# Optimization experiments

Measured on AMD Instinct MI355X. Metric: run time of the kernel, lower is better.

## Reference

```python
import jax, jax.numpy as jnp
import numpy as np

N = 100000          # nodes
E = 1_600_000       # edges (nnz of sparse adj)
IN_F = 256
OUT_F = 128
DROP_P = 0.2


def setup_inputs() -> dict:
    key = jax.random.key(0)
    k1, k2, k3, k4, k5, k6 = jax.random.split(key, 6)
    return {
        "input": jax.random.normal(k1, (N, IN_F), dtype=jnp.float32),
        "weight": jax.random.normal(k2, (IN_F, OUT_F), dtype=jnp.float32) * 0.05,
        "adj_row": jax.random.randint(k3, (E,), 0, N, dtype=jnp.int32),
        "adj_col": jax.random.randint(k4, (E,), 0, N, dtype=jnp.int32),
        "adj_val": jax.random.uniform(k5, (E,), dtype=jnp.float32),
        "drop_u": jax.random.uniform(k6, (N, IN_F), dtype=jnp.float32),
    }


def reference(input, weight, adj_row, adj_col, adj_val, drop_u):
    # F.dropout(input, p, training=True): zero with prob p, scale survivors by 1/(1-p)
    x = jnp.where(drop_u > DROP_P, input / (1.0 - DROP_P), 0.0)
    # dense projection: [N, in] @ [in, out] -> [N, out]
    support = x @ weight
    # SpMM: out[r] = sum over edges e with row==r of val[e] * support[col[e]]
    gathered = support[adj_col] * adj_val[:, None]          # [E, out]
    output = jax.ops.segment_sum(gathered, adj_row, num_segments=N)  # [N, out]
    return output
```

## Files before the change

### kernel.cpp

```cpp
#include <hip/hip_runtime.h>

#define N_NODES 100000
#define IN_F 256
#define OUT_F 128
#define NB 782
#define CAP 2560
#define TILE 4096

typedef __attribute__((ext_vector_type(8))) short v8s;
typedef __attribute__((ext_vector_type(4))) float v4f;

__device__ __forceinline__ unsigned short f2bf(float f) {
    unsigned int u = __float_as_uint(f);
    u += 0x7fffu + ((u >> 16) & 1u);
    return (unsigned short)(u >> 16);
}
__device__ __forceinline__ float bf2f(unsigned short s) {
    return __uint_as_float((unsigned int)s << 16);
}

__global__ __launch_bounds__(256) void drop_kernel(
    const float* __restrict__ x, const float* __restrict__ u,
    unsigned short* __restrict__ xb, int n4) {
    int i = blockIdx.x * 256 + threadIdx.x;
    int stride = gridDim.x * 256;
    for (; i < n4; i += stride) {
        float4 xi = ((const float4*)x)[i];
        float4 du = ((const float4*)u)[i];
        ushort4 pk;
        pk.x = f2bf(du.x > 0.2f ? xi.x * 1.25f : 0.0f);
        pk.y = f2bf(du.y > 0.2f ? xi.y * 1.25f : 0.0f);
        pk.z = f2bf(du.z > 0.2f ? xi.z * 1.25f : 0.0f);
        pk.w = f2bf(du.w > 0.2f ? xi.w * 1.25f : 0.0f);
        ((ushort4*)xb)[i] = pk;
    }
}

__global__ void wt_kernel(const float* __restrict__ w, unsigned short* __restrict__ bt) {
    int idx = blockIdx.x * 256 + threadIdx.x;
    int k = idx >> 7;
    int n = idx & 127;
    bt[n * IN_F + k] = f2bf(w[idx]);
}

__global__ __launch_bounds__(256) void gemm_kernel(
    const unsigned short* __restrict__ xb, const unsigned short* __restrict__ bt,
    unsigned short* __restrict__ support) {
    __shared__ unsigned short As[128 * 72];
    __shared__ unsigned short Bs[128 * 72];

    const int tid  = threadIdx.x;
    const int lane = tid & 63;
    const int wv   = tid >> 6;
    const int wr   = wv >> 1, wc = wv & 1;
    const long long base = (long long)blockIdx.x * 128;

    v4f acc[4][4] = {};

    for (int k0 = 0; k0 < IN_F; k0 += 64) {
        if (k0) __syncthreads();
        {
            const int row = tid >> 1;
            const int kh  = (tid & 1) * 32;
            long long g = base + row;
            unsigned short* dst = &As[row * 72 + kh];
            if (g < N_NODES) {
                const unsigned short* src = xb + g * IN_F + k0 + kh;
                #pragma unroll
                for (int i = 0; i < 4; ++i)
                    *(v8s*)(dst + i * 8) = *(const v8s*)(src + i * 8);
            } else {
                #pragma unroll
                for (int i = 0; i < 4; ++i)
                    *(v8s*)(dst + i * 8) = (v8s){0,0,0,0,0,0,0,0};
            }
        }
        {
            const int n  = tid >> 1;
            const int kh = (tid & 1) * 32;
            const unsigned short* src = bt + n * IN_F + k0 + kh;
            unsigned short* dst = &Bs[n * 72 + kh];
            #pragma unroll
            for (int i = 0; i < 4; ++i)
                *(v8s*)(dst + i * 8) = *(const v8s*)(src + i * 8);
        }
        __syncthreads();
        #pragma unroll
        for (int ks = 0; ks < 2; ++ks) {
            const int kb = ks * 32 + (lane >> 4) * 8;
            v8s af[4], bf[4];
            #pragma unroll
            for (int t = 0; t < 4; ++t)
                af[t] = *(const v8s*)&As[(wr * 64 + t * 16 + (lane & 15)) * 72 + kb];
            #pragma unroll
            for (int t = 0; t < 4; ++t)
                bf[t] = *(const v8s*)&Bs[(wc * 64 + t * 16 + (lane & 15)) * 72 + kb];
            #pragma unroll
            for (int tm = 0; tm < 4; ++tm)
                #pragma unroll
                for (int tn = 0; tn < 4; ++tn)
                    acc[tm][tn] = __builtin_amdgcn_mfma_f32_16x16x32_bf16(
                        af[tm], bf[tn], acc[tm][tn], 0, 0, 0);
        }
    }
    const int rq = lane >> 4;
    const int cl = lane & 15;
    #pragma unroll
    for (int tm = 0; tm < 4; ++tm) {
        #pragma unroll
        for (int r = 0; r < 4; ++r) {
            long long g = base + wr * 64 + tm * 16 + rq * 4 + r;
            if (g < N_NODES) {
                unsigned short* o = support + g * OUT_F + wc * 64 + cl;
                #pragma unroll
                for (int tn = 0; tn < 4; ++tn)
                    o[tn * 16] = f2bf(acc[tm][tn][r]);
            }
        }
    }
}

__global__ void init_kernel(int* __restrict__ cursor) {
    int i = blockIdx.x * 256 + threadIdx.x;
    if (i < NB) cursor[i * 16] = i * CAP;
}

__global__ __launch_bounds__(256) void scatter_kernel(
    const int* __restrict__ row, const int* __restrict__ col,
    const float* __restrict__ val, int* __restrict__ cursor,
    int2* __restrict__ cv, int E) {
    __shared__ int cnt[1024];
    __shared__ int loc[1024];
    __shared__ int delta[1024];
    __shared__ int tmp[256];
    __shared__ int gd[TILE];
    __shared__ int2 stage[TILE];
    __shared__ int total_s;
    const int tid = threadIdx.x;
    const int base_e = blockIdx.x * TILE;

    for (int i = tid; i < 1024; i += 256) cnt[i] = 0;
    __syncthreads();
    #pragma unroll
    for (int j = 0; j < TILE / 256; ++j) {
        int e = base_e + j * 256 + tid;
        if (e < E) atomicAdd(&cnt[row[e] >> 7], 1);
    }
    __syncthreads();
    int c0 = cnt[4*tid], c1 = cnt[4*tid+1], c2 = cnt[4*tid+2], c3 = cnt[4*tid+3];
    int s = c0 + c1 + c2 + c3;
    tmp[tid] = s;
    __syncthreads();
    #pragma unroll
    for (int d = 1; d < 256; d <<= 1) {
        int t = (tid >= d) ? tmp[tid - d] : 0;
        __syncthreads();
        tmp[tid] += t;
        __syncthreads();
    }
    int excl = tmp[tid] - s;
    loc[4*tid]   = excl;
    loc[4*tid+1] = excl + c0;
    loc[4*tid+2] = excl + c0 + c1;
    loc[4*tid+3] = excl + c0 + c1 + c2;
    if (tid == 255) total_s = tmp[255];
    __syncthreads();
    for (int i = tid; i < NB; i += 256) {
        int c = cnt[i];
        int gbase = 0;
        if (c > 0) gbase = atomicAdd(&cursor[i * 16], c);
        delta[i] = gbase - loc[i];
        cnt[i] = loc[i];
    }
    __syncthreads();
    #pragma unroll
    for (int j = 0; j < TILE / 256; ++j) {
        int e = base_e + j * 256 + tid;
        if (e < E) {
            int r = row[e];
            int b = r >> 7;
            int rank = atomicAdd(&cnt[b], 1);
            stage[rank] = make_int2(col[e] | ((r & 127) << 17), __float_as_int(val[e]));
            gd[rank] = delta[b] + rank;
        }
    }
    __syncthreads();
    int total = total_s;
    for (int i = tid; i < total; i += 256)
        cv[gd[i]] = stage[i];
}

__global__ __launch_bounds__(256) void acc2_kernel(
    const int* __restrict__ cursor, const int2* __restrict__ cv,
    const unsigned short* __restrict__ support, float* __restrict__ out) {
    __shared__ int2 sorted[CAP];
    __shared__ int cnt_s[128];
    __shared__ int start_s[128];
    __shared__ int pos_s[128];
    const int tid = threadIdx.x;
    const int b = blockIdx.x;
    const int e0 = b * CAP;
    const int nE = cursor[b * 16] - e0;

    if (tid < 128) cnt_s[tid] = 0;
    __syncthreads();
    for (int i = tid; i < nE; i += 256)
        atomicAdd(&cnt_s[cv[e0 + i].x >> 17], 1);
    __syncthreads();
    int v = (tid < 128) ? cnt_s[tid] : 0;
    int sc = v;
    if (tid < 128) pos_s[tid] = sc;
    __syncthreads();
    #pragma unroll
    for (int d = 1; d < 128; d <<= 1) {
        int t = (tid >= d && tid < 128) ? pos_s[tid - d] : 0;
        __syncthreads();
        if (tid < 128) pos_s[tid] += t;
        __syncthreads();
    }
    if (tid < 128) {
        int st = pos_s[tid] - v;
        start_s[tid] = st;
        pos_s[tid] = st;
    }
    __syncthreads();
    for (int i = tid; i < nE; i += 256) {
        int2 c = cv[e0 + i];
        int rank = atomicAdd(&pos_s[c.x >> 17], 1);
        sorted[rank] = c;
    }
    __syncthreads();
    const int lane = tid & 63, w = tid >> 6;
    const long long rowbase = (long long)b * 128;
    for (int rr = 0; rr < 32; ++rr) {
        int rl = w * 32 + rr;
        int e = start_s[rl];
        int end = e + cnt_s[rl];
        float a0 = 0.f, a1 = 0.f;
        for (; e < end; e += 4) {
            #pragma unroll
            for (int j = 0; j < 4; ++j) {
                int idx = e + j;
                int ids = min(idx, end - 1);
                int2 c = sorted[ids];
                float vv = (idx < end) ? __int_as_float(c.y) : 0.0f;
                int colv = c.x & 131071;
                unsigned int u = *(const unsigned int*)(support + colv * OUT_F + lane * 2);
                a0 = fmaf(vv, bf2f((unsigned short)(u & 0xffff)), a0);
                a1 = fmaf(vv, bf2f((unsigned short)(u >> 16)), a1);
            }
        }
        long long g = rowbase + rl;
        if (g < N_NODES)
            *(float2*)(out + g * OUT_F + lane * 2) = make_float2(a0, a1);
    }
}

extern "C" void kernel_launch(void* const* d_in, const int* in_sizes, int n_in,
                              void* d_out, int out_size, void* d_ws, size_t ws_size,
                              hipStream_t stream) {
    const float* input   = (const float*)d_in[0];
    const float* weight  = (const float*)d_in[1];
    const int*   adj_row = (const int*)d_in[2];
    const int*   adj_col = (const int*)d_in[3];
    const float* adj_val = (const float*)d_in[4];
    const float* drop_u  = (const float*)d_in[5];
    float* out = (float*)d_out;
    const int E = in_sizes[2];

    char* p = (char*)d_ws;
    unsigned short* bt      = (unsigned short*)p;  p += 65536;
    unsigned short* xb      = (unsigned short*)p;
    int2*           cv      = (int2*)p;            p += (size_t)N_NODES * IN_F * 2;
    unsigned short* support = (unsigned short*)p;  p += (size_t)N_NODES * OUT_F * 2;
    int*            cursor  = (int*)p;

    init_kernel<<<4, 256, 0, stream>>>(cursor);
    drop_kernel<<<2048, 256, 0, stream>>>(input, drop_u, xb, N_NODES * IN_F / 4);
    wt_kernel<<<128, 256, 0, stream>>>(weight, bt);
    gemm_kernel<<<(N_NODES + 127) / 128, 256, 0, stream>>>(xb, bt, support);
    scatter_kernel<<<(E + TILE - 1) / TILE, 256, 0, stream>>>(adj_row, adj_col, adj_val, cursor, cv, E);
    acc2_kernel<<<NB, 256, 0, stream>>>(cursor, cv, support, out);
}
```

Measured before the change: 424.7 us.

## Fuse dropout into GEMM load and split SpMM accumulation across four blocks per bucket

The separate dropout kernel is removed. The GEMM now reads fp32 input and dropout uniforms directly, applies the mask and scale, and packs to bf16 while filling shared memory. This avoids a full bf16 intermediate write and read of the dropped input. The accumulation kernel launches four blocks per 128-row bucket, each handling 32 rows with smaller shared memory and a warp-shuffle scan, which raises parallelism and occupancy. In exchange, each block rereads the whole bucket's edge list and filters it, and the GEMM tile load now issues twice as many fp32 reads.

```diff
diff --git a/kernel.cpp b/kernel.cpp
--- a/kernel.cpp
+++ b/kernel.cpp
@@ -5,6 +5,7 @@
 #define OUT_F 128
 #define NB 782
 #define CAP 2560
+#define QCAP 896
 #define TILE 4096
 
 typedef __attribute__((ext_vector_type(8))) short v8s;
@@ -17,23 +18,6 @@
 }
 __device__ __forceinline__ float bf2f(unsigned short s) {
     return __uint_as_float((unsigned int)s << 16);
-}
-
-__global__ __launch_bounds__(256) void drop_kernel(
-    const float* __restrict__ x, const float* __restrict__ u,
-    unsigned short* __restrict__ xb, int n4) {
-    int i = blockIdx.x * 256 + threadIdx.x;
-    int stride = gridDim.x * 256;
-    for (; i < n4; i += stride) {
-        float4 xi = ((const float4*)x)[i];
-        float4 du = ((const float4*)u)[i];
-        ushort4 pk;
-        pk.x = f2bf(du.x > 0.2f ? xi.x * 1.25f : 0.0f);
-        pk.y = f2bf(du.y > 0.2f ? xi.y * 1.25f : 0.0f);
-        pk.z = f2bf(du.z > 0.2f ? xi.z * 1.25f : 0.0f);
-        pk.w = f2bf(du.w > 0.2f ? xi.w * 1.25f : 0.0f);
-        ((ushort4*)xb)[i] = pk;
-    }
 }
 
 __global__ void wt_kernel(const float* __restrict__ w, unsigned short* __restrict__ bt) {
@@ -44,8 +28,8 @@
 }
 
 __global__ __launch_bounds__(256) void gemm_kernel(
-    const unsigned short* __restrict__ xb, const unsigned short* __restrict__ bt,
-    unsigned short* __restrict__ support) {
+    const float* __restrict__ x, const float* __restrict__ u,
+    const unsigned short* __restrict__ bt, unsigned short* __restrict__ support) {
     __shared__ unsigned short As[128 * 72];
     __shared__ unsigned short Bs[128 * 72];
 
@@ -65,10 +49,19 @@
             long long g = base + row;
             unsigned short* dst = &As[row * 72 + kh];
             if (g < N_NODES) {
-                const unsigned short* src = xb + g * IN_F + k0 + kh;
-                #pragma unroll
-                for (int i = 0; i < 4; ++i)
-                    *(v8s*)(dst + i * 8) = *(const v8s*)(src + i * 8);
+                const float* xs = x + g * IN_F + k0 + kh;
+                const float* us = u + g * IN_F + k0 + kh;
+                #pragma unroll
+                for (int i = 0; i < 8; ++i) {
+                    float4 xi = *(const float4*)(xs + i * 4);
+                    float4 du = *(const float4*)(us + i * 4);
+                    ushort4 pk;
+                    pk.x = f2bf(du.x > 0.2f ? xi.x * 1.25f : 0.0f);
+                    pk.y = f2bf(du.y > 0.2f ? xi.y * 1.25f : 0.0f);
+                    pk.z = f2bf(du.z > 0.2f ? xi.z * 1.25f : 0.0f);
+                    pk.w = f2bf(du.w > 0.2f ? xi.w * 1.25f : 0.0f);
+                    *(ushort4*)(dst + i * 4) = pk;
+                }
             } else {
                 #pragma unroll
                 for (int i = 0; i < 4; ++i)
@@ -193,47 +186,50 @@
 __global__ __launch_bounds__(256) void acc2_kernel(
     const int* __restrict__ cursor, const int2* __restrict__ cv,
     const unsigned short* __restrict__ support, float* __restrict__ out) {
-    __shared__ int2 sorted[CAP];
-    __shared__ int cnt_s[128];
-    __shared__ int start_s[128];
-    __shared__ int pos_s[128];
+    __shared__ int2 sorted[QCAP];
+    __shared__ int cnt_s[32];
+    __shared__ int start_s[32];
+    __shared__ int pos_s[32];
     const int tid = threadIdx.x;
-    const int b = blockIdx.x;
+    const int bq = blockIdx.x;
+    const int b = bq >> 2;
+    const int q = bq & 3;
     const int e0 = b * CAP;
     const int nE = cursor[b * 16] - e0;
 
-    if (tid < 128) cnt_s[tid] = 0;
-    __syncthreads();
-    for (int i = tid; i < nE; i += 256)
-        atomicAdd(&cnt_s[cv[e0 + i].x >> 17], 1);
-    __syncthreads();
-    int v = (tid < 128) ? cnt_s[tid] : 0;
-    int sc = v;
-    if (tid < 128) pos_s[tid] = sc;
-    __syncthreads();
-    #pragma unroll
-    for (int d = 1; d < 128; d <<= 1) {
-        int t = (tid >= d && tid < 128) ? pos_s[tid - d] : 0;
-        __syncthreads();
-        if (tid < 128) pos_s[tid] += t;
-        __syncthreads();
-    }
-    if (tid < 128) {
-        int st = pos_s[tid] - v;
-        start_s[tid] = st;
-        pos_s[tid] = st;
+    if (tid < 32) cnt_s[tid] = 0;
+    __syncthreads();
+    for (int i = tid; i < nE; i += 256) {
+        int cx = cv[e0 + i].x;
+        int lr = cx >> 17;
+        if ((lr >> 5) == q) atomicAdd(&cnt_s[lr & 31], 1);
+    }
+    __syncthreads();
+    if (tid < 32) {
+        int v = cnt_s[tid];
+        int sc = v;
+        #pragma unroll
+        for (int d = 1; d < 32; d <<= 1) {
+            int t = __shfl_up(sc, d, 64);
+            if (tid >= d) sc += t;
+        }
+        start_s[tid] = sc - v;
+        pos_s[tid] = sc - v;
     }
     __syncthreads();
     for (int i = tid; i < nE; i += 256) {
         int2 c = cv[e0 + i];
-        int rank = atomicAdd(&pos_s[c.x >> 17], 1);
-        sorted[rank] = c;
+        int lr = c.x >> 17;
+        if ((lr >> 5) == q) {
+            int rank = atomicAdd(&pos_s[lr & 31], 1);
+            sorted[rank] = c;
+        }
     }
     __syncthreads();
     const int lane = tid & 63, w = tid >> 6;
-    const long long rowbase = (long long)b * 128;
-    for (int rr = 0; rr < 32; ++rr) {
-        int rl = w * 32 + rr;
+    const long long rowbase = (long long)b * 128 + q * 32;
+    for (int rr = 0; rr < 8; ++rr) {
+        int rl = w * 8 + rr;
         int e = start_s[rl];
         int end = e + cnt_s[rl];
         float a0 = 0.f, a1 = 0.f;
@@ -245,9 +241,9 @@
                 int2 c = sorted[ids];
                 float vv = (idx < end) ? __int_as_float(c.y) : 0.0f;
                 int colv = c.x & 131071;
-                unsigned int u = *(const unsigned int*)(support + colv * OUT_F + lane * 2);
-                a0 = fmaf(vv, bf2f((unsigned short)(u & 0xffff)), a0);
-                a1 = fmaf(vv, bf2f((unsigned short)(u >> 16)), a1);
+                unsigned int uu = *(const unsigned int*)(support + colv * OUT_F + lane * 2);
+                a0 = fmaf(vv, bf2f((unsigned short)(uu & 0xffff)), a0);
+                a1 = fmaf(vv, bf2f((unsigned short)(uu >> 16)), a1);
             }
         }
         long long g = rowbase + rl;
@@ -270,15 +266,13 @@
 
     char* p = (char*)d_ws;
     unsigned short* bt      = (unsigned short*)p;  p += 65536;
-    unsigned short* xb      = (unsigned short*)p;
-    int2*           cv      = (int2*)p;            p += (size_t)N_NODES * IN_F * 2;
+    int2*           cv      = (int2*)p;            p += (size_t)NB * CAP * sizeof(int2);
     unsigned short* support = (unsigned short*)p;  p += (size_t)N_NODES * OUT_F * 2;
     int*            cursor  = (int*)p;
 
     init_kernel<<<4, 256, 0, stream>>>(cursor);
-    drop_kernel<<<2048, 256, 0, stream>>>(input, drop_u, xb, N_NODES * IN_F / 4);
     wt_kernel<<<128, 256, 0, stream>>>(weight, bt);
-    gemm_kernel<<<(N_NODES + 127) / 128, 256, 0, stream>>>(xb, bt, support);
+    gemm_kernel<<<(N_NODES + 127) / 128, 256, 0, stream>>>(input, drop_u, bt, support);
     scatter_kernel<<<(E + TILE - 1) / TILE, 256, 0, stream>>>(adj_row, adj_col, adj_val, cursor, cv, E);
-    acc2_kernel<<<NB, 256, 0, stream>>>(cursor, cv, support, out);
-}
+    acc2_kernel<<<NB * 4, 256, 0, stream>>>(cursor, cv, support, out);
+}
```

Measured after the change: 393.5 us. 7.3% less time.
